# Performance work log

Measured on AMD Instinct MI355X. Metric: run time of the kernel, lower is better.

The kernel has to match this reference:

```python
import jax, jax.numpy as jnp
import numpy as np

B, M, D, H = 2, 2048, 1024, 16


def _rope(x):
    # Equivalent to x.transpose(0,1) @ R[:m] with R the block-diagonal 2x2
    # rotation matrices from get_rotary_matrix (note the (i-1) in theta,
    # faithful to the source).
    b, m, d = x.shape
    i = jnp.arange(d // 2, dtype=jnp.float32)
    theta = 10000.0 ** (-2.0 * (i - 1.0) / d)           # [d/2]
    ang = jnp.arange(m, dtype=jnp.float32)[:, None] * theta[None, :]  # [m, d/2]
    c, s = jnp.cos(ang), jnp.sin(ang)
    xe, xo = x[..., 0::2], x[..., 1::2]                 # [b, m, d/2]
    ye = xe * c + xo * s                                # out[2i]   = q[2i]*cos + q[2i+1]*sin
    yo = -xe * s + xo * c                               # out[2i+1] = -q[2i]*sin + q[2i+1]*cos
    return jnp.stack([ye, yo], axis=-1).reshape(b, m, d)


def setup_inputs() -> dict:
    key = jax.random.key(0)
    ks = jax.random.split(key, 8)
    w = lambda k, shape: (jax.random.normal(k, shape, jnp.float32) * 0.02)
    return {
        "x": jax.random.normal(ks[0], (B, M, D), jnp.float32),
        "wq": w(ks[1], (D, D)),
        "wk": w(ks[2], (D, D)),
        "wv": w(ks[3], (D, D)),
        "in_proj_w": w(ks[4], (3 * D, D)),
        "in_proj_b": w(ks[5], (3 * D,)),
        "out_w": w(ks[6], (D, D)),
        "out_b": w(ks[7], (D,)),
    }


def reference(x, wq, wk, wv, in_proj_w, in_proj_b, out_w, out_b):
    b, m, d = x.shape
    h = H
    hd = d // h
    # bias-free QKV projections, each followed by the dense RoPE rotation
    q = _rope(x @ wq.T)
    k = _rope(x @ wk.T)
    v = _rope(x @ wv.T)
    # nn.MultiheadAttention: packed in_proj, scaled dot-product, causal mask, out_proj
    wqi, wki, wvi = jnp.split(in_proj_w, 3, axis=0)
    bqi, bki, bvi = jnp.split(in_proj_b, 3, axis=0)
    qh = (q @ wqi.T + bqi).reshape(b, m, h, hd)
    kh = (k @ wki.T + bki).reshape(b, m, h, hd)
    vh = (v @ wvi.T + bvi).reshape(b, m, h, hd)
    scores = jnp.einsum("bqhd,bkhd->bhqk", qh, kh) / jnp.sqrt(jnp.float32(hd))
    causal = jnp.tril(jnp.ones((m, m), dtype=bool))
    scores = jnp.where(causal, scores, jnp.float32(-jnp.inf))
    attn = jax.nn.softmax(scores, axis=-1)              # dropout p=0.0
    o = jnp.einsum("bhqk,bkhd->bqhd", attn, vh).reshape(b, m, d)
    return o @ out_w.T + out_b
```

## Files before the change

kernel.cpp:

```cpp
#include <hip/hip_runtime.h>
#include <hip/hip_bf16.h>
#include <math.h>

typedef __bf16 bf16;
typedef __bf16 bf16x4 __attribute__((ext_vector_type(4)));
typedef __bf16 bf16x8 __attribute__((ext_vector_type(8)));
typedef float  f32x4  __attribute__((ext_vector_type(4)));

#define MM 2048
#define DD 1024
#define HD 64

__device__ __forceinline__ void gload16(const void* g, void* l) {
  __builtin_amdgcn_global_load_lds((const __attribute__((address_space(1))) void*)g,
                                   (__attribute__((address_space(3))) void*)l, 16, 0, 0);
}

__global__ __launch_bounds__(256) void k_cvt_all(
    const float* __restrict__ x,   const float* __restrict__ wq,
    const float* __restrict__ wk,  const float* __restrict__ wv,
    const float* __restrict__ ipw, const float* __restrict__ ow,
    bf16* __restrict__ xb,  bf16* __restrict__ wqb, bf16* __restrict__ wkb,
    bf16* __restrict__ wvb, bf16* __restrict__ ipwb, bf16* __restrict__ owb)
{
  int bid = blockIdx.x;
  const float* s; bf16* d; int base;
  if (bid < 4096)       { s = x;   d = xb;   base = bid; }
  else if (bid < 5120)  { s = wq;  d = wqb;  base = bid - 4096; }
  else if (bid < 6144)  { s = wk;  d = wkb;  base = bid - 5120; }
  else if (bid < 7168)  { s = wv;  d = wvb;  base = bid - 6144; }
  else if (bid < 10240) { s = ipw; d = ipwb; base = bid - 7168; }
  else                  { s = ow;  d = owb;  base = bid - 10240; }
  int i = base*256 + threadIdx.x;
  float4 v = ((const float4*)s)[i];
  bf16x4 o;
  o[0]=(bf16)v.x; o[1]=(bf16)v.y; o[2]=(bf16)v.z; o[3]=(bf16)v.w;
  ((bf16x4*)d)[i] = o;
}

__device__ __forceinline__ void gemm_core(const bf16* __restrict__ A,
                                          const bf16* __restrict__ Bw,
                                          const int row0, const int col0,
                                          bf16* __restrict__ sA, bf16* __restrict__ sB,
                                          f32x4 (&acc)[4][4])
{
  const int t = threadIdx.x;
  #pragma unroll
  for (int m=0;m<4;m++)
    #pragma unroll
    for (int n=0;n<4;n++)
      acc[m][n] = (f32x4){0.f,0.f,0.f,0.f};

  const int srow = t >> 3;
  const int lch  = ((t & 7) - (srow & 7)) & 7;
  const bf16* gA = A  + (size_t)(row0 + srow)*DD + lch*8;
  const bf16* gB = Bw + (size_t)(col0 + srow)*DD + lch*8;
  char* lA = (char*)sA + t*16;
  char* lB = (char*)sB + t*16;

  const int lane = t & 63, wid = t >> 6;
  const int wr = wid >> 1, wc = wid & 1;
  const int fr = lane & 15, fg = lane >> 4;
  const int fr7 = fr & 7;

  #pragma unroll
  for (int jj=0;jj<4;jj++) gload16(gA + (size_t)jj*32*DD, lA + jj*4096);
  #pragma unroll
  for (int jj=0;jj<4;jj++) gload16(gB + (size_t)jj*32*DD, lB + jj*4096);

  for (int kt = 0; kt < 16; ++kt) {
    const int buf = kt & 1;
    __builtin_amdgcn_s_barrier();
    if (kt < 15) {
      const int nb = buf ^ 1;
      const int ko = (kt + 1) * 64;
      #pragma unroll
      for (int jj=0;jj<4;jj++) gload16(gA + (size_t)jj*32*DD + ko, lA + nb*16384 + jj*4096);
      #pragma unroll
      for (int jj=0;jj<4;jj++) gload16(gB + (size_t)jj*32*DD + ko, lB + nb*16384 + jj*4096);
      asm volatile("s_waitcnt vmcnt(8)" ::: "memory");
    } else {
      asm volatile("s_waitcnt vmcnt(0)" ::: "memory");
    }
    __builtin_amdgcn_s_barrier();
    const char* bA = (const char*)sA + buf*16384;
    const char* bB = (const char*)sB + buf*16384;
    bf16x8 aF[2][4], bF[2][4];
    #pragma unroll
    for (int kb=0;kb<2;kb++) {
      #pragma unroll
      for (int m=0;m<4;m++)
        aF[kb][m] = *(const bf16x8*)(bA + (wr*64 + m*16 + fr)*128 + ((kb*4 + fg + fr7)&7)*16);
      #pragma unroll
      for (int n=0;n<4;n++)
        bF[kb][n] = *(const bf16x8*)(bB + (wc*64 + n*16 + fr)*128 + ((kb*4 + fg + fr7)&7)*16);
    }
    __builtin_amdgcn_s_setprio(1);
    #pragma unroll
    for (int kb=0;kb<2;kb++)
      #pragma unroll
      for (int m=0;m<4;m++)
        #pragma unroll
        for (int n=0;n<4;n++)
          acc[m][n] = __builtin_amdgcn_mfma_f32_16x16x32_bf16(aF[kb][m], bF[kb][n], acc[m][n], 0, 0, 0);
    __builtin_amdgcn_s_setprio(0);
  }
}

__global__ __launch_bounds__(256, 2) void k_gemm_rope(
    const bf16* __restrict__ X, const bf16* __restrict__ Wq,
    const bf16* __restrict__ Wk, const bf16* __restrict__ Wv,
    bf16* __restrict__ QKV)
{
  __shared__ bf16 sA[2*128*64];
  __shared__ bf16 sB[2*128*64];
  const int row0 = blockIdx.x * 128;
  const int col0 = blockIdx.y * 128;
  const int z = blockIdx.z;
  const bf16* Bw = (z==0) ? Wq : ((z==1) ? Wk : Wv);
  f32x4 acc[4][4];
  gemm_core(X, Bw, row0, col0, sA, sB, acc);

  bf16* outp = QKV + (size_t)z * (4096u*1024u);
  const int lane = threadIdx.x & 63, wid = threadIdx.x >> 6;
  const int wr = wid >> 1, wc = wid & 1;
  const int fr = lane & 15, fg = lane >> 4;
  #pragma unroll
  for (int n=0;n<4;n++) {
    const int gc = col0 + wc*64 + n*16 + fr;
    const int i2 = gc >> 1;
    const float theta = __expf(((float)i2 - 1.0f) * (-2.0f * 9.210340371976184f / 1024.0f));
    #pragma unroll
    for (int m=0;m<4;m++) {
      #pragma unroll
      for (int r=0;r<4;r++) {
        const int gr = row0 + wr*64 + m*16 + fg*4 + r;
        const float v  = acc[m][n][r];
        const float pv = __shfl_xor(v, 1);
        const int pos = gr & (MM-1);
        float sv, cv;
        __sincosf((float)pos * theta, &sv, &cv);
        const float res = (gc & 1) ? (v*cv - pv*sv) : (v*cv + pv*sv);
        outp[(size_t)gr * DD + gc] = (bf16)res;
      }
    }
  }
}

__global__ __launch_bounds__(256, 2) void k_gemm_proj(
    const bf16* __restrict__ QKV, const bf16* __restrict__ IPW,
    const float* __restrict__ IPB,
    bf16* __restrict__ QH, bf16* __restrict__ KH, bf16* __restrict__ VT)
{
  __shared__ bf16 sA[2*128*64];
  __shared__ bf16 sB[2*128*64];
  const int row0 = blockIdx.x * 128;
  const int col0 = blockIdx.y * 128;
  const int z = blockIdx.z;
  const bf16* A  = QKV + (size_t)z * (4096u*1024u);
  const bf16* Bw = IPW + (size_t)z * (1024u*1024u);
  const float* bias = IPB + z * DD;
  f32x4 acc[4][4];
  gemm_core(A, Bw, row0, col0, sA, sB, acc);

  const int lane = threadIdx.x & 63, wid = threadIdx.x >> 6;
  const int wr = wid >> 1, wc = wid & 1;
  const int fr = lane & 15, fg = lane >> 4;
  if (z < 2) {
    bf16* outp = (z==0) ? QH : KH;
    const float vscale = (z==0) ? 0.125f : 1.0f;
    #pragma unroll
    for (int n=0;n<4;n++) {
      const int gc = col0 + wc*64 + n*16 + fr;
      const float bs = bias[gc];
      #pragma unroll
      for (int m=0;m<4;m++) {
        #pragma unroll
        for (int r=0;r<4;r++) {
          const int gr = row0 + wr*64 + m*16 + fg*4 + r;
          outp[(size_t)gr * DD + gc] = (bf16)((acc[m][n][r] + bs) * vscale);
        }
      }
    }
  } else {
    #pragma unroll
    for (int n=0;n<4;n++) {
      const int gc = col0 + wc*64 + n*16 + fr;
      const float bs = bias[gc];
      #pragma unroll
      for (int m=0;m<4;m++) {
        const int gr0 = row0 + wr*64 + m*16 + fg*4;
        const int b  = gr0 >> 11;
        const int m0 = gr0 & (MM-1);
        bf16x4 pk;
        #pragma unroll
        for (int r=0;r<4;r++) pk[r] = (bf16)(acc[m][n][r] + bs);
        *(bf16x4*)(VT + ((size_t)b*DD + gc)*MM + m0) = pk;
      }
    }
  }
}

__global__ __launch_bounds__(256) void k_attn(
    const bf16* __restrict__ QH, const bf16* __restrict__ KH,
    const bf16* __restrict__ VT, bf16* __restrict__ O)
{
  __shared__ bf16 sK[3*64*64];
  __shared__ bf16 sV[3*64*64];
  __shared__ bf16 sP[4*16*64];
  const int idx = blockIdx.x;
  const int xcd = idx & 7;
  const int rr  = idx >> 3;
  const int combo = xcd*4 + (rr & 3);
  const int b = combo >> 4, h = combo & 15;
  const int pair = rr >> 2;
  const int t = threadIdx.x, lane = t & 63, wid = t >> 6;
  const int fr = lane & 15, fg = lane >> 4;
  const int swzP = (fr & 7) << 4;

  const int srow = t >> 3;
  const int cc   = (t & 7) ^ (srow & 7);
  const bf16* gK0 = KH + ((size_t)b*MM + srow)*DD + h*HD + cc*8;
  const bf16* gK1 = gK0 + (size_t)32*DD;
  const bf16* gV0 = VT + ((size_t)b*DD + h*HD + srow)*MM + cc*8;
  const bf16* gV1 = gV0 + (size_t)32*MM;
  char* lK = (char*)sK + t*16;
  char* lV = (char*)sV + t*16;
  char* sPw = (char*)(sP + wid*16*64);

  #pragma unroll 1
  for (int half = 0; half < 2; ++half) {
    const int qt = half ? pair : (31 - pair);
    const int q0 = qt * 64;
    const int qg = q0 + wid*16 + fr;

    const bf16* qp = QH + ((size_t)b*MM + qg)*DD + h*HD + fg*8;
    bf16x8 aQ0 = *(const bf16x8*)qp;
    bf16x8 aQ1 = *(const bf16x8*)(qp + 32);

    if (half) __builtin_amdgcn_s_barrier();

    gload16(gK0, lK);  gload16(gK1, lK + 4096);
    gload16(gV0, lV);  gload16(gV1, lV + 4096);
    if (qt >= 1) {
      gload16(gK0 + (size_t)64*DD, lK + 8192);
      gload16(gK1 + (size_t)64*DD, lK + 8192 + 4096);
      gload16(gV0 + 64, lV + 8192);
      gload16(gV1 + 64, lV + 8192 + 4096);
    }

    f32x4 o_acc[4];
    #pragma unroll
    for (int n=0;n<4;n++) o_acc[n] = (f32x4){0.f,0.f,0.f,0.f};
    float mrow = -INFINITY, lrow = 0.f;

    int c = 0;
    for (int kt = 0; kt <= qt; ++kt) {
      if (kt < qt) asm volatile("s_waitcnt vmcnt(4)" ::: "memory");
      else         asm volatile("s_waitcnt vmcnt(0)" ::: "memory");
      __builtin_amdgcn_s_barrier();
      if (kt + 2 <= qt) {
        const int nb = (c + 2 < 3) ? c + 2 : c - 1;
        gload16(gK0 + (size_t)(kt+2)*64*DD, lK + nb*8192);
        gload16(gK1 + (size_t)(kt+2)*64*DD, lK + nb*8192 + 4096);
        gload16(gV0 + (kt+2)*64,            lV + nb*8192);
        gload16(gV1 + (kt+2)*64,            lV + nb*8192 + 4096);
      }
      const char* bKb = (const char*)sK + c*8192;
      const char* bVb = (const char*)sV + c*8192;

      f32x4 sacc[4];
      #pragma unroll
      for (int n=0;n<4;n++) sacc[n] = (f32x4){0.f,0.f,0.f,0.f};
      __builtin_amdgcn_s_setprio(1);
      #pragma unroll
      for (int kb=0;kb<2;kb++) {
        const bf16x8 q = kb ? aQ1 : aQ0;
        #pragma unroll
        for (int n=0;n<4;n++) {
          const int rowA = n*16 + fr;
          bf16x8 aK = *(const bf16x8*)(bKb + rowA*128 + ((kb*64 + fg*16) ^ ((rowA&7)<<4)));
          sacc[n] = __builtin_amdgcn_mfma_f32_16x16x32_bf16(aK, q, sacc[n], 0, 0, 0);
        }
      }
      __builtin_amdgcn_s_setprio(0);

      const bool diag = (kt == qt);
      float pv[16];
      #pragma unroll
      for (int n=0;n<4;n++)
        #pragma unroll
        for (int r=0;r<4;r++) {
          float xx = sacc[n][r];
          if (diag) {
            const int kvg = kt*64 + n*16 + fg*4 + r;
            if (kvg > qg) xx = -INFINITY;
          }
          pv[n*4+r] = xx;
        }
      float m8[8];
      #pragma unroll
      for (int i=0;i<8;i++) m8[i] = fmaxf(pv[i], pv[i+8]);
      #pragma unroll
      for (int i=0;i<4;i++) m8[i] = fmaxf(m8[i], m8[i+4]);
      float rmax = fmaxf(fmaxf(m8[0],m8[1]), fmaxf(m8[2],m8[3]));
      rmax = fmaxf(rmax, __shfl_xor(rmax, 16));
      rmax = fmaxf(rmax, __shfl_xor(rmax, 32));
      if (!__all(rmax - mrow <= 8.f)) {
        const float mnew = fmaxf(mrow, rmax);
        const float scale = __expf(mrow - mnew);
        mrow = mnew;
        lrow *= scale;
        float sc[4];
        #pragma unroll
        for (int r=0;r<4;r++) sc[r] = __shfl(scale, fg*4 + r);
        #pragma unroll
        for (int n=0;n<4;n++)
          #pragma unroll
          for (int r=0;r<4;r++) o_acc[n][r] *= sc[r];
      }
      float ps[16];
      #pragma unroll
      for (int i=0;i<16;i++) ps[i] = __expf(pv[i] - mrow);
      #pragma unroll
      for (int n=0;n<4;n++) {
        bf16x4 pk;
        #pragma unroll
        for (int r=0;r<4;r++) pk[r] = (bf16)ps[n*4+r];
        *(bf16x4*)(sPw + fr*128 + ((n*32 + fg*8) ^ swzP)) = pk;
      }
      float s8[8];
      #pragma unroll
      for (int i=0;i<8;i++) s8[i] = ps[i] + ps[i+8];
      #pragma unroll
      for (int i=0;i<4;i++) s8[i] += s8[i+4];
      float rsum = (s8[0]+s8[1]) + (s8[2]+s8[3]);
      rsum += __shfl_xor(rsum, 16);
      rsum += __shfl_xor(rsum, 32);
      lrow += rsum;
      asm volatile("s_waitcnt lgkmcnt(0)" ::: "memory");

      bf16x8 aP0 = *(const bf16x8*)(sPw + fr*128 + ((fg*16) ^ swzP));
      bf16x8 aP1 = *(const bf16x8*)(sPw + fr*128 + ((64 + fg*16) ^ swzP));
      __builtin_amdgcn_s_setprio(1);
      #pragma unroll
      for (int n=0;n<4;n++) {
        const int rowV = n*16 + fr;
        bf16x8 bV0 = *(const bf16x8*)(bVb + rowV*128 + ((fg*16) ^ ((rowV&7)<<4)));
        bf16x8 bV1 = *(const bf16x8*)(bVb + rowV*128 + ((64 + fg*16) ^ ((rowV&7)<<4)));
        o_acc[n] = __builtin_amdgcn_mfma_f32_16x16x32_bf16(aP0, bV0, o_acc[n], 0, 0, 0);
        o_acc[n] = __builtin_amdgcn_mfma_f32_16x16x32_bf16(aP1, bV1, o_acc[n], 0, 0, 0);
      }
      __builtin_amdgcn_s_setprio(0);
      c = (c == 2) ? 0 : c + 1;
    }

    const float linv = 1.0f / lrow;
    float inv4[4];
    #pragma unroll
    for (int r=0;r<4;r++) inv4[r] = __shfl(linv, fg*4 + r);
    #pragma unroll
    for (int r=0;r<4;r++) {
      const int qq = q0 + wid*16 + fg*4 + r;
      #pragma unroll
      for (int n=0;n<4;n++) {
        O[((size_t)b*MM + qq)*DD + h*HD + n*16 + fr] = (bf16)(o_acc[n][r] * inv4[r]);
      }
    }
  }
}

__global__ __launch_bounds__(256, 2) void k_gemm_out(
    const bf16* __restrict__ A, const bf16* __restrict__ OW,
    const float* __restrict__ OBIAS, float* __restrict__ outp)
{
  __shared__ bf16 sA[2*128*64];
  __shared__ bf16 sB[2*128*64];
  const int row0 = blockIdx.x * 128;
  const int col0 = blockIdx.y * 128;
  f32x4 acc[4][4];
  gemm_core(A, OW, row0, col0, sA, sB, acc);
  const int lane = threadIdx.x & 63, wid = threadIdx.x >> 6;
  const int wr = wid >> 1, wc = wid & 1;
  const int fr = lane & 15, fg = lane >> 4;
  #pragma unroll
  for (int n=0;n<4;n++) {
    const int gc = col0 + wc*64 + n*16 + fr;
    const float bs = OBIAS[gc];
    #pragma unroll
    for (int m=0;m<4;m++) {
      #pragma unroll
      for (int r=0;r<4;r++) {
        const int gr = row0 + wr*64 + m*16 + fg*4 + r;
        outp[(size_t)gr * DD + gc] = acc[m][n][r] + bs;
      }
    }
  }
}

extern "C" void kernel_launch(void* const* d_in, const int* in_sizes, int n_in,
                              void* d_out, int out_size, void* d_ws, size_t ws_size,
                              hipStream_t stream)
{
  (void)in_sizes; (void)n_in; (void)out_size; (void)ws_size;
  const float* x   = (const float*)d_in[0];
  const float* wq  = (const float*)d_in[1];
  const float* wk  = (const float*)d_in[2];
  const float* wv  = (const float*)d_in[3];
  const float* ipw = (const float*)d_in[4];
  const float* ipb = (const float*)d_in[5];
  const float* ow  = (const float*)d_in[6];
  const float* ob  = (const float*)d_in[7];
  float* outp = (float*)d_out;

  char* ws = (char*)d_ws;
  const size_t MB = 1u << 20;
  bf16* xb   = (bf16*)(ws + 0*MB);
  bf16* wqb  = (bf16*)(ws + 8*MB);
  bf16* wkb  = (bf16*)(ws + 10*MB);
  bf16* wvb  = (bf16*)(ws + 12*MB);
  bf16* ipwb = (bf16*)(ws + 14*MB);
  bf16* owb  = (bf16*)(ws + 20*MB);
  bf16* QKV  = (bf16*)(ws + 22*MB);
  bf16* QH   = (bf16*)(ws + 46*MB);
  bf16* KH   = (bf16*)(ws + 54*MB);
  bf16* VT   = (bf16*)(ws + 62*MB);
  bf16* Ob   = (bf16*)(ws + 70*MB);

  k_cvt_all<<<11264, 256, 0, stream>>>(x, wq, wk, wv, ipw, ow,
                                       xb, wqb, wkb, wvb, ipwb, owb);
  k_gemm_rope<<<dim3(32,8,3), 256, 0, stream>>>(xb, wqb, wkb, wvb, QKV);
  k_gemm_proj<<<dim3(32,8,3), 256, 0, stream>>>(QKV, ipwb, ipb, QH, KH, VT);
  k_attn<<<512, 256, 0, stream>>>(QH, KH, VT, Ob);
  k_gemm_out<<<dim3(32,8,1), 256, 0, stream>>>(Ob, owb, ob, outp);
}
```

Baseline: 154.4 us.

## Widen attention KV tiles to 128 with double buffering, use exp2, remap GEMM blocks

The attention kernel now processes 128-key tiles with a two-stage buffer instead of 64-key tiles with a three-stage ring, so there are fewer barriers and online-softmax steps per query tile. Softmax switches to exp2f, with the log2(e) factor folded into the Q scale, and the rescale threshold is raised. The GEMM kernels remap the flat block index so that consecutive blocks share a row tile across column groups, aiming at better cache locality. In exchange, the diagonal tile masks more wasted work at 128 granularity, register pressure rises, and prefetch overlap drops to a single stage.

Measured after the change: 172.2 us. 11.5% more time.

```diff
diff --git a/kernel.cpp b/kernel.cpp
--- a/kernel.cpp
+++ b/kernel.cpp
@@ -114,9 +114,12 @@
 {
   __shared__ bf16 sA[2*128*64];
   __shared__ bf16 sB[2*128*64];
-  const int row0 = blockIdx.x * 128;
-  const int col0 = blockIdx.y * 128;
-  const int z = blockIdx.z;
+  const int fl = blockIdx.x + 32*(blockIdx.y + 8*blockIdx.z);
+  const int cg = fl & 7;
+  const int rest = fl >> 3;
+  const int row0 = (rest & 31) * 128;
+  const int col0 = cg * 128;
+  const int z = rest >> 5;
   const bf16* Bw = (z==0) ? Wq : ((z==1) ? Wk : Wv);
   f32x4 acc[4][4];
   gemm_core(X, Bw, row0, col0, sA, sB, acc);
@@ -154,9 +157,12 @@
 {
   __shared__ bf16 sA[2*128*64];
   __shared__ bf16 sB[2*128*64];
-  const int row0 = blockIdx.x * 128;
-  const int col0 = blockIdx.y * 128;
-  const int z = blockIdx.z;
+  const int fl = blockIdx.x + 32*(blockIdx.y + 8*blockIdx.z);
+  const int cg = fl & 7;
+  const int rest = fl >> 3;
+  const int row0 = (rest & 31) * 128;
+  const int col0 = cg * 128;
+  const int z = rest >> 5;
   const bf16* A  = QKV + (size_t)z * (4096u*1024u);
   const bf16* Bw = IPW + (size_t)z * (1024u*1024u);
   const float* bias = IPB + z * DD;
@@ -168,7 +174,7 @@
   const int fr = lane & 15, fg = lane >> 4;
   if (z < 2) {
     bf16* outp = (z==0) ? QH : KH;
-    const float vscale = (z==0) ? 0.125f : 1.0f;
+    const float vscale = (z==0) ? 0.18033688011112042f : 1.0f;
     #pragma unroll
     for (int n=0;n<4;n++) {
       const int gc = col0 + wc*64 + n*16 + fr;
@@ -205,9 +211,9 @@
     const bf16* __restrict__ QH, const bf16* __restrict__ KH,
     const bf16* __restrict__ VT, bf16* __restrict__ O)
 {
-  __shared__ bf16 sK[3*64*64];
-  __shared__ bf16 sV[3*64*64];
-  __shared__ bf16 sP[4*16*64];
+  __shared__ bf16 sK[2*128*64];
+  __shared__ bf16 sV[2*64*128];
+  __shared__ bf16 sP[4*16*128];
   const int idx = blockIdx.x;
   const int xcd = idx & 7;
   const int rr  = idx >> 3;
@@ -216,23 +222,24 @@
   const int pair = rr >> 2;
   const int t = threadIdx.x, lane = t & 63, wid = t >> 6;
   const int fr = lane & 15, fg = lane >> 4;
-  const int swzP = (fr & 7) << 4;
-
-  const int srow = t >> 3;
-  const int cc   = (t & 7) ^ (srow & 7);
-  const bf16* gK0 = KH + ((size_t)b*MM + srow)*DD + h*HD + cc*8;
-  const bf16* gK1 = gK0 + (size_t)32*DD;
-  const bf16* gV0 = VT + ((size_t)b*DD + h*HD + srow)*MM + cc*8;
-  const bf16* gV1 = gV0 + (size_t)32*MM;
+  const int fr7 = fr & 7;
+
+  const int krow = t >> 3;
+  const int kcc  = (t & 7) ^ (krow & 7);
+  const bf16* gK = KH + ((size_t)b*MM + krow)*DD + h*HD + kcc*8;
+  const int vrow = t >> 4;
+  const int vcc  = (t & 15) ^ (vrow & 7);
+  const bf16* gV = VT + ((size_t)b*DD + h*HD + vrow)*MM + vcc*8;
   char* lK = (char*)sK + t*16;
   char* lV = (char*)sV + t*16;
-  char* sPw = (char*)(sP + wid*16*64);
+  char* sPw = (char*)sP + wid*4096;
 
   #pragma unroll 1
   for (int half = 0; half < 2; ++half) {
     const int qt = half ? pair : (31 - pair);
     const int q0 = qt * 64;
     const int qg = q0 + wid*16 + fr;
+    const int ntiles = (qt + 2) >> 1;
 
     const bf16* qp = QH + ((size_t)b*MM + qg)*DD + h*HD + fg*8;
     bf16x8 aQ0 = *(const bf16x8*)qp;
@@ -240,75 +247,74 @@
 
     if (half) __builtin_amdgcn_s_barrier();
 
-    gload16(gK0, lK);  gload16(gK1, lK + 4096);
-    gload16(gV0, lV);  gload16(gV1, lV + 4096);
-    if (qt >= 1) {
-      gload16(gK0 + (size_t)64*DD, lK + 8192);
-      gload16(gK1 + (size_t)64*DD, lK + 8192 + 4096);
-      gload16(gV0 + 64, lV + 8192);
-      gload16(gV1 + 64, lV + 8192 + 4096);
-    }
+    #pragma unroll
+    for (int j=0;j<4;j++) gload16(gK + (size_t)j*32*DD, lK + j*4096);
+    #pragma unroll
+    for (int j=0;j<4;j++) gload16(gV + (size_t)j*16*MM, lV + j*4096);
 
     f32x4 o_acc[4];
     #pragma unroll
     for (int n=0;n<4;n++) o_acc[n] = (f32x4){0.f,0.f,0.f,0.f};
     float mrow = -INFINITY, lrow = 0.f;
 
-    int c = 0;
-    for (int kt = 0; kt <= qt; ++kt) {
-      if (kt < qt) asm volatile("s_waitcnt vmcnt(4)" ::: "memory");
-      else         asm volatile("s_waitcnt vmcnt(0)" ::: "memory");
+    for (int kt = 0; kt < ntiles; ++kt) {
+      const int buf = kt & 1;
+      asm volatile("s_waitcnt vmcnt(0)" ::: "memory");
       __builtin_amdgcn_s_barrier();
-      if (kt + 2 <= qt) {
-        const int nb = (c + 2 < 3) ? c + 2 : c - 1;
-        gload16(gK0 + (size_t)(kt+2)*64*DD, lK + nb*8192);
-        gload16(gK1 + (size_t)(kt+2)*64*DD, lK + nb*8192 + 4096);
-        gload16(gV0 + (kt+2)*64,            lV + nb*8192);
-        gload16(gV1 + (kt+2)*64,            lV + nb*8192 + 4096);
-      }
-      const char* bKb = (const char*)sK + c*8192;
-      const char* bVb = (const char*)sV + c*8192;
-
-      f32x4 sacc[4];
-      #pragma unroll
-      for (int n=0;n<4;n++) sacc[n] = (f32x4){0.f,0.f,0.f,0.f};
+      if (kt + 1 < ntiles) {
+        const int nb = buf ^ 1;
+        const size_t ko = (size_t)(kt+1) * 128 * DD;
+        const int vo = (kt+1) * 128;
+        #pragma unroll
+        for (int j=0;j<4;j++) gload16(gK + ko + (size_t)j*32*DD, lK + nb*16384 + j*4096);
+        #pragma unroll
+        for (int j=0;j<4;j++) gload16(gV + vo + (size_t)j*16*MM, lV + nb*16384 + j*4096);
+      }
+      const char* bKb = (const char*)sK + buf*16384;
+      const char* bVb = (const char*)sV + buf*16384;
+
+      f32x4 sacc[8];
+      #pragma unroll
+      for (int n=0;n<8;n++) sacc[n] = (f32x4){0.f,0.f,0.f,0.f};
       __builtin_amdgcn_s_setprio(1);
       #pragma unroll
       for (int kb=0;kb<2;kb++) {
         const bf16x8 q = kb ? aQ1 : aQ0;
         #pragma unroll
-        for (int n=0;n<4;n++) {
+        for (int n=0;n<8;n++) {
           const int rowA = n*16 + fr;
-          bf16x8 aK = *(const bf16x8*)(bKb + rowA*128 + ((kb*64 + fg*16) ^ ((rowA&7)<<4)));
+          bf16x8 aK = *(const bf16x8*)(bKb + rowA*128 + (((kb*4 + fg) ^ (rowA&7))*16));
           sacc[n] = __builtin_amdgcn_mfma_f32_16x16x32_bf16(aK, q, sacc[n], 0, 0, 0);
         }
       }
       __builtin_amdgcn_s_setprio(0);
 
-      const bool diag = (kt == qt);
-      float pv[16];
-      #pragma unroll
-      for (int n=0;n<4;n++)
+      const bool diag = (kt == ntiles - 1);
+      float pv[32];
+      #pragma unroll
+      for (int n=0;n<8;n++)
         #pragma unroll
         for (int r=0;r<4;r++) {
           float xx = sacc[n][r];
           if (diag) {
-            const int kvg = kt*64 + n*16 + fg*4 + r;
+            const int kvg = kt*128 + n*16 + fg*4 + r;
             if (kvg > qg) xx = -INFINITY;
           }
           pv[n*4+r] = xx;
         }
-      float m8[8];
-      #pragma unroll
-      for (int i=0;i<8;i++) m8[i] = fmaxf(pv[i], pv[i+8]);
-      #pragma unroll
-      for (int i=0;i<4;i++) m8[i] = fmaxf(m8[i], m8[i+4]);
-      float rmax = fmaxf(fmaxf(m8[0],m8[1]), fmaxf(m8[2],m8[3]));
+      float mmx[16];
+      #pragma unroll
+      for (int i=0;i<16;i++) mmx[i] = fmaxf(pv[i], pv[i+16]);
+      #pragma unroll
+      for (int i=0;i<8;i++) mmx[i] = fmaxf(mmx[i], mmx[i+8]);
+      #pragma unroll
+      for (int i=0;i<4;i++) mmx[i] = fmaxf(mmx[i], mmx[i+4]);
+      float rmax = fmaxf(fmaxf(mmx[0],mmx[1]), fmaxf(mmx[2],mmx[3]));
       rmax = fmaxf(rmax, __shfl_xor(rmax, 16));
       rmax = fmaxf(rmax, __shfl_xor(rmax, 32));
-      if (!__all(rmax - mrow <= 8.f)) {
+      if (!__all(rmax - mrow <= 11.5f)) {
         const float mnew = fmaxf(mrow, rmax);
-        const float scale = __expf(mrow - mnew);
+        const float scale = exp2f(mrow - mnew);
         mrow = mnew;
         lrow *= scale;
         float sc[4];
@@ -319,40 +325,43 @@
           #pragma unroll
           for (int r=0;r<4;r++) o_acc[n][r] *= sc[r];
       }
-      float ps[16];
-      #pragma unroll
-      for (int i=0;i<16;i++) ps[i] = __expf(pv[i] - mrow);
-      #pragma unroll
-      for (int n=0;n<4;n++) {
+      #pragma unroll
+      for (int i=0;i<32;i++) pv[i] = exp2f(pv[i] - mrow);
+      #pragma unroll
+      for (int n=0;n<8;n++) {
         bf16x4 pk;
         #pragma unroll
-        for (int r=0;r<4;r++) pk[r] = (bf16)ps[n*4+r];
-        *(bf16x4*)(sPw + fr*128 + ((n*32 + fg*8) ^ swzP)) = pk;
-      }
-      float s8[8];
-      #pragma unroll
-      for (int i=0;i<8;i++) s8[i] = ps[i] + ps[i+8];
-      #pragma unroll
-      for (int i=0;i<4;i++) s8[i] += s8[i+4];
-      float rsum = (s8[0]+s8[1]) + (s8[2]+s8[3]);
+        for (int r=0;r<4;r++) pk[r] = (bf16)pv[n*4+r];
+        *(bf16x4*)(sPw + fr*256 + ((n*32 + fg*8) ^ (fr7<<4))) = pk;
+      }
+      float s16[16];
+      #pragma unroll
+      for (int i=0;i<16;i++) s16[i] = pv[i] + pv[i+16];
+      #pragma unroll
+      for (int i=0;i<8;i++) s16[i] += s16[i+8];
+      #pragma unroll
+      for (int i=0;i<4;i++) s16[i] += s16[i+4];
+      float rsum = (s16[0]+s16[1]) + (s16[2]+s16[3]);
       rsum += __shfl_xor(rsum, 16);
       rsum += __shfl_xor(rsum, 32);
       lrow += rsum;
       asm volatile("s_waitcnt lgkmcnt(0)" ::: "memory");
 
-      bf16x8 aP0 = *(const bf16x8*)(sPw + fr*128 + ((fg*16) ^ swzP));
-      bf16x8 aP1 = *(const bf16x8*)(sPw + fr*128 + ((64 + fg*16) ^ swzP));
+      bf16x8 aP[4];
+      #pragma unroll
+      for (int ks=0;ks<4;ks++)
+        aP[ks] = *(const bf16x8*)(sPw + fr*256 + ((ks*64 + fg*16) ^ (fr7<<4)));
       __builtin_amdgcn_s_setprio(1);
       #pragma unroll
       for (int n=0;n<4;n++) {
         const int rowV = n*16 + fr;
-        bf16x8 bV0 = *(const bf16x8*)(bVb + rowV*128 + ((fg*16) ^ ((rowV&7)<<4)));
-        bf16x8 bV1 = *(const bf16x8*)(bVb + rowV*128 + ((64 + fg*16) ^ ((rowV&7)<<4)));
-        o_acc[n] = __builtin_amdgcn_mfma_f32_16x16x32_bf16(aP0, bV0, o_acc[n], 0, 0, 0);
-        o_acc[n] = __builtin_amdgcn_mfma_f32_16x16x32_bf16(aP1, bV1, o_acc[n], 0, 0, 0);
+        #pragma unroll
+        for (int ks=0;ks<4;ks++) {
+          bf16x8 bV = *(const bf16x8*)(bVb + rowV*256 + (((ks*4 + fg) ^ (rowV&7))*16));
+          o_acc[n] = __builtin_amdgcn_mfma_f32_16x16x32_bf16(aP[ks], bV, o_acc[n], 0, 0, 0);
+        }
       }
       __builtin_amdgcn_s_setprio(0);
-      c = (c == 2) ? 0 : c + 1;
     }
 
     const float linv = 1.0f / lrow;
@@ -376,8 +385,10 @@
 {
   __shared__ bf16 sA[2*128*64];
   __shared__ bf16 sB[2*128*64];
-  const int row0 = blockIdx.x * 128;
-  const int col0 = blockIdx.y * 128;
+  const int fl = blockIdx.x + 32*blockIdx.y;
+  const int cg = fl & 7;
+  const int row0 = (fl >> 3) * 128;
+  const int col0 = cg * 128;
   f32x4 acc[4][4];
   gemm_core(A, OW, row0, col0, sA, sB, acc);
   const int lane = threadIdx.x & 63, wid = threadIdx.x >> 6;
```
